# Performance work log

Measured on AMD Instinct MI355X. Metric: run time of the kernel, lower is better.

The kernel has to match this reference:

```python
import jax, jax.numpy as jnp
import numpy as np

P = 16         # patch size
D = 192        # embed dim (vit_tiny)
NH = 3         # heads
DEPTH = 12
HID = 768      # mlp hidden = 4*D
NCLS = 1000
PCT = 0.25
EPS = 1e-6


def _ln(x, s, b):
    m = x.mean(-1, keepdims=True)
    v = ((x - m) ** 2).mean(-1, keepdims=True)
    return (x - m) * jax.lax.rsqrt(v + EPS) * s + b


def setup_inputs() -> dict:
    key = jax.random.key(0)
    ks = jax.random.split(key, 24)
    B, IMG = 64, 384
    std = 0.02
    d = {
        "magno_image": jax.random.normal(ks[0], (B, 3, IMG, IMG), jnp.float32),
        "line_drawing": jax.random.uniform(ks[1], (B, 1, IMG, IMG), jnp.float32),
        "conv_w": jax.random.normal(ks[2], (D, 3, P, P), jnp.float32) * std,
        "conv_b": jnp.zeros((D,), jnp.float32),
        "pos_embed": jax.random.normal(ks[3], (1, (IMG // P) ** 2 + 1, D), jnp.float32) * std,
        "cls_token": jax.random.normal(ks[4], (1, 1, D), jnp.float32) * std,
        "ln1_s": jnp.ones((DEPTH, D), jnp.float32),
        "ln1_b": jnp.zeros((DEPTH, D), jnp.float32),
        "qkv_w": jax.random.normal(ks[5], (DEPTH, D, 3 * D), jnp.float32) * std,
        "qkv_b": jnp.zeros((DEPTH, 3 * D), jnp.float32),
        "proj_w": jax.random.normal(ks[6], (DEPTH, D, D), jnp.float32) * std,
        "proj_b": jnp.zeros((DEPTH, D), jnp.float32),
        "ln2_s": jnp.ones((DEPTH, D), jnp.float32),
        "ln2_b": jnp.zeros((DEPTH, D), jnp.float32),
        "fc1_w": jax.random.normal(ks[7], (DEPTH, D, HID), jnp.float32) * std,
        "fc1_b": jnp.zeros((DEPTH, HID), jnp.float32),
        "fc2_w": jax.random.normal(ks[8], (DEPTH, HID, D), jnp.float32) * std,
        "fc2_b": jnp.zeros((DEPTH, D), jnp.float32),
        "normf_s": jnp.ones((D,), jnp.float32),
        "normf_b": jnp.zeros((D,), jnp.float32),
        "head_w": jax.random.normal(ks[9], (D, NCLS), jnp.float32) * std,
        "head_b": jnp.zeros((NCLS,), jnp.float32),
    }
    return d


def _forward(magno_image, line_drawing, conv_w, conv_b, pos_embed, cls_token,
             ln1_s, ln1_b, qkv_w, qkv_b, proj_w, proj_b, ln2_s, ln2_b,
             fc1_w, fc1_b, fc2_w, fc2_b, normf_s, normf_b, head_w, head_b):
    B, _, IMG, _ = magno_image.shape
    g = IMG // P
    N = g * g
    k = int(N * PCT)
    hd = D // NH

    # --- PatchImportanceScorer: avg-pool(patch_size) then flatten ---
    scores = line_drawing.reshape(B, g, P, g, P).mean(axis=(2, 4)).reshape(B, N)

    # --- patch embed (conv stride == kernel == reshaped matmul) ---
    x = magno_image.reshape(B, 3, g, P, g, P).transpose(0, 2, 4, 1, 3, 5)
    patches = x.reshape(B, N, 3 * P * P) @ conv_w.reshape(D, 3 * P * P).T + conv_b

    # --- top_k selection + gather of patches and pos-embed ---
    _, idx = jax.lax.top_k(scores, k)                      # (B, k)
    sel = jnp.take_along_axis(patches, idx[:, :, None], axis=1)
    pos = jnp.take_along_axis(
        jnp.broadcast_to(pos_embed[:, 1:, :], (B, N, D)), idx[:, :, None], axis=1)
    sel = sel + pos

    cls = jnp.broadcast_to(cls_token + pos_embed[:, :1, :], (B, 1, D))
    seq = jnp.concatenate([cls, sel], axis=1)              # (B, 1+k, D)
    S = 1 + k

    def block(h, p):
        l1s, l1b, qw, qb, pw, pb, l2s, l2b, f1w, f1b, f2w, f2b = p
        y = _ln(h, l1s, l1b)
        qkv = (y @ qw + qb).reshape(B, S, 3, NH, hd)
        q, kk, v = qkv[:, :, 0], qkv[:, :, 1], qkv[:, :, 2]  # (B,S,NH,hd)
        att = jnp.einsum('bqhd,bkhd->bhqk', q, kk) / np.sqrt(hd).astype(np.float32)
        att = jax.nn.softmax(att, axis=-1)
        o = jnp.einsum('bhqk,bkhd->bqhd', att, v).reshape(B, S, D)
        h = h + o @ pw + pb
        y = _ln(h, l2s, l2b)
        h = h + jax.nn.gelu(y @ f1w + f1b, approximate=False) @ f2w + f2b
        return h, None

    seq, _ = jax.lax.scan(block, seq, (ln1_s, ln1_b, qkv_w, qkv_b, proj_w, proj_b,
                                       ln2_s, ln2_b, fc1_w, fc1_b, fc2_w, fc2_b))
    seq = _ln(seq, normf_s, normf_b)
    return seq[:, 0] @ head_w + head_b


def reference(magno_image, line_drawing, conv_w, conv_b, pos_embed, cls_token,
              ln1_s, ln1_b, qkv_w, qkv_b, proj_w, proj_b, ln2_s, ln2_b,
              fc1_w, fc1_b, fc2_w, fc2_b, normf_s, normf_b, head_w, head_b):
    return _forward(magno_image, line_drawing, conv_w, conv_b, pos_embed, cls_token,
                    ln1_s, ln1_b, qkv_w, qkv_b, proj_w, proj_b, ln2_s, ln2_b,
                    fc1_w, fc1_b, fc2_w, fc2_b, normf_s, normf_b, head_w, head_b)
```

## Files before the change

### kernel.cpp

```cpp
#include <hip/hip_runtime.h>
#include <hip/hip_bf16.h>
#include <cmath>


#define Bsz   64
#define NPATCH 576
#define KSEL  144
#define SEQ   145
#define DIM   192
#define HIDN  768

typedef __bf16 bf16x8 __attribute__((ext_vector_type(8)));
typedef float  f32x4  __attribute__((ext_vector_type(4)));

__global__ __launch_bounds__(256) void scores_kernel(const float* __restrict__ line,
                                                     float* __restrict__ scores)
{
    int gp = blockIdx.x;
    int b = gp / NPATCH, p = gp % NPATCH;
    int gy = p / 24, gx = p % 24;
    int t = threadIdx.x, py = t >> 4, px = t & 15;
    float v = line[((size_t)b * 384 + gy * 16 + py) * 384 + gx * 16 + px];
    for (int off = 32; off; off >>= 1) v += __shfl_xor(v, off);
    __shared__ float red[4];
    if ((t & 63) == 0) red[t >> 6] = v;
    __syncthreads();
    if (t == 0) scores[gp] = (red[0] + red[1] + red[2] + red[3]) * (1.f / 256.f);
}

__global__ __launch_bounds__(256) void topk_kernel(const float* __restrict__ scores,
                                                   int* __restrict__ idx)
{
    int b = blockIdx.x;
    __shared__ float s[NPATCH];
    for (int i = threadIdx.x; i < NPATCH; i += 256) s[i] = scores[b * NPATCH + i];
    __syncthreads();
    for (int i = threadIdx.x; i < NPATCH; i += 256) {
        float si = s[i];
        int cnt = 0;
        for (int j = 0; j < NPATCH; ++j) {
            float sj = s[j];
            cnt += (sj > si) || (sj == si && j < i);
        }
        if (cnt < KSEL) idx[b * KSEL + cnt] = i;
    }
}

__global__ __launch_bounds__(256) void gather_kernel(const float* __restrict__ magno,
                                                     const int* __restrict__ idx,
                                                     __hip_bfloat16* __restrict__ selp)
{
    int bs = blockIdx.x;
    int b = bs / KSEL;
    int pi = idx[bs];
    int gy = pi / 24, gx = pi % 24;
    int t = threadIdx.x, py = t >> 4, px = t & 15;
    size_t src = ((size_t)b * 3 * 384 + gy * 16 + py) * 384 + gx * 16 + px;
    __hip_bfloat16* dst = &selp[(size_t)bs * 768];
#pragma unroll
    for (int c = 0; c < 3; ++c)
        dst[c * 256 + t] = __float2bfloat16(magno[src + (size_t)c * 384 * 384]);
}

__global__ __launch_bounds__(256) void convert_bf16_kernel(const float* __restrict__ src,
                                                           __hip_bfloat16* __restrict__ dst,
                                                           int n)
{
    int i = blockIdx.x * 256 + threadIdx.x;
    if (i < n) dst[i] = __float2bfloat16(src[i]);
}

__global__ __launch_bounds__(256) void transpose_w_kernel(const float* __restrict__ src,
                                                          __hip_bfloat16* __restrict__ dst,
                                                          int R, int C)
{
    __shared__ float t[32][33];
    size_t lo = (size_t)blockIdx.z * R * C;
    int r0 = blockIdx.y * 32, c0 = blockIdx.x * 32;
    int tx = threadIdx.x & 31, ty = threadIdx.x >> 5;
#pragma unroll
    for (int i = 0; i < 32; i += 8)
        t[ty + i][tx] = src[lo + (size_t)(r0 + ty + i) * C + c0 + tx];
    __syncthreads();
#pragma unroll
    for (int i = 0; i < 32; i += 8)
        dst[lo + (size_t)(c0 + ty + i) * R + r0 + tx] = __float2bfloat16(t[tx][ty + i]);
}

__global__ void cls_kernel(const float* __restrict__ cls, const float* __restrict__ pos,
                           float* __restrict__ h)
{
    int b = blockIdx.x, t = threadIdx.x;
    h[(size_t)b * SEQ * DIM + t] = cls[t] + pos[t];
}

__global__ __launch_bounds__(256) void ln_kernel(const float* __restrict__ x,
                                                 const float* __restrict__ s,
                                                 const float* __restrict__ bia,
                                                 __hip_bfloat16* __restrict__ y, int ntok)
{
    int w = threadIdx.x >> 6, lane = threadIdx.x & 63;
    int tok = blockIdx.x * 4 + w;
    if (tok >= ntok) return;
    const float* xp = &x[(size_t)tok * DIM];
    float x0 = xp[lane], x1 = xp[lane + 64], x2 = xp[lane + 128];
    float sum = x0 + x1 + x2;
    for (int off = 32; off; off >>= 1) sum += __shfl_xor(sum, off);
    float mean = sum * (1.f / 192.f);
    float d0 = x0 - mean, d1 = x1 - mean, d2 = x2 - mean;
    float vs = d0 * d0 + d1 * d1 + d2 * d2;
    for (int off = 32; off; off >>= 1) vs += __shfl_xor(vs, off);
    float rs = rsqrtf(vs * (1.f / 192.f) + 1e-6f);
    __hip_bfloat16* yp = &y[(size_t)tok * DIM];
    yp[lane]       = __float2bfloat16(d0 * rs * s[lane]       + bia[lane]);
    yp[lane + 64]  = __float2bfloat16(d1 * rs * s[lane + 64]  + bia[lane + 64]);
    yp[lane + 128] = __float2bfloat16(d2 * rs * s[lane + 128] + bia[lane + 128]);
}

template <int MODE>
__global__ __launch_bounds__(256) void gemm_bf16(const __hip_bfloat16* __restrict__ A,
                                                 const __hip_bfloat16* __restrict__ Wt,
                                                 const float* __restrict__ bias,
                                                 void* __restrict__ Cout,
                                                 int M, int N, int K,
                                                 const int* __restrict__ selidx,
                                                 const float* __restrict__ pos)
{
    __shared__ __align__(16) char As[8192];
    __shared__ __align__(16) char Bs[8192];
    const int tid = threadIdx.x;
    const int lane = tid & 63, wid = tid >> 6;
    const int wr = wid >> 1, wc = wid & 1;
    const int lr = lane & 15, lk = lane >> 4;
    const int m0 = blockIdx.y * 64, n0 = blockIdx.x * 64;
    f32x4 acc[2][2] = {};

    for (int k0 = 0; k0 < K; k0 += 64) {
#pragma unroll
        for (int it = 0; it < 2; ++it) {
            int chunk = it * 256 + tid;
            int r = chunk >> 3, g = chunk & 7;
            int loff = r * 128 + ((g ^ (r & 7)) * 16);
            *reinterpret_cast<uint4*>(As + loff) =
                *reinterpret_cast<const uint4*>(&A[(size_t)(m0 + r) * K + k0 + g * 8]);
            *reinterpret_cast<uint4*>(Bs + loff) =
                *reinterpret_cast<const uint4*>(&Wt[(size_t)(n0 + r) * K + k0 + g * 8]);
        }
        __syncthreads();
#pragma unroll
        for (int kc = 0; kc < 2; ++kc) {
            int g = kc * 4 + lk;
            bf16x8 af[2], bfr[2];
#pragma unroll
            for (int mi = 0; mi < 2; ++mi) {
                int r = wr * 32 + mi * 16 + lr;
                af[mi] = *reinterpret_cast<const bf16x8*>(As + r * 128 + ((g ^ (r & 7)) * 16));
            }
#pragma unroll
            for (int ni = 0; ni < 2; ++ni) {
                int r = wc * 32 + ni * 16 + lr;
                bfr[ni] = *reinterpret_cast<const bf16x8*>(Bs + r * 128 + ((g ^ (r & 7)) * 16));
            }
#pragma unroll
            for (int mi = 0; mi < 2; ++mi)
#pragma unroll
                for (int ni = 0; ni < 2; ++ni)
                    acc[mi][ni] = __builtin_amdgcn_mfma_f32_16x16x32_bf16(
                        af[mi], bfr[ni], acc[mi][ni], 0, 0, 0);
        }
        __syncthreads();
    }

#pragma unroll
    for (int mi = 0; mi < 2; ++mi)
#pragma unroll
    for (int ni = 0; ni < 2; ++ni)
#pragma unroll
    for (int j = 0; j < 4; ++j) {
        int row = m0 + wr * 32 + mi * 16 + (lane >> 4) * 4 + j;
        int col = n0 + wc * 32 + ni * 16 + (lane & 15);
        float v = acc[mi][ni][j] + bias[col];
        if (MODE == 2) {
            ((__hip_bfloat16*)Cout)[(size_t)row * N + col] =
                __float2bfloat16(0.5f * v * (1.f + erff(v * 0.70710678118654752f)));
        } else {
            int bb2 = row / KSEL, ss = row % KSEL;
            int pi = selidx[row];
            v += pos[(size_t)(1 + pi) * DIM + col];
            ((float*)Cout)[((size_t)bb2 * SEQ + 1 + ss) * DIM + col] = v;
        }
    }
}

__global__ __launch_bounds__(256) void gemm_qkv(const __hip_bfloat16* __restrict__ A,
                                                const __hip_bfloat16* __restrict__ Wt,
                                                const float* __restrict__ bias,
                                                __hip_bfloat16* __restrict__ qk,
                                                __hip_bfloat16* __restrict__ Vt)
{
    __shared__ __align__(16) char As[8192];
    __shared__ __align__(16) char Bs[8192];
    const int tid = threadIdx.x;
    const int lane = tid & 63, wid = tid >> 6;
    const int wr = wid >> 1, wc = wid & 1;
    const int lr = lane & 15, lk = lane >> 4;
    const int m0 = blockIdx.y * 64, n0 = blockIdx.x * 64;
    const int K = DIM;
    f32x4 acc[2][2] = {};

    for (int k0 = 0; k0 < K; k0 += 64) {
#pragma unroll
        for (int it = 0; it < 2; ++it) {
            int chunk = it * 256 + tid;
            int r = chunk >> 3, g = chunk & 7;
            int loff = r * 128 + ((g ^ (r & 7)) * 16);
            *reinterpret_cast<uint4*>(As + loff) =
                *reinterpret_cast<const uint4*>(&A[(size_t)(m0 + r) * K + k0 + g * 8]);
            *reinterpret_cast<uint4*>(Bs + loff) =
                *reinterpret_cast<const uint4*>(&Wt[(size_t)(n0 + r) * K + k0 + g * 8]);
        }
        __syncthreads();
#pragma unroll
        for (int kc = 0; kc < 2; ++kc) {
            int g = kc * 4 + lk;
            bf16x8 af[2], bfr[2];
#pragma unroll
            for (int mi = 0; mi < 2; ++mi) {
                int r = wr * 32 + mi * 16 + lr;
                af[mi] = *reinterpret_cast<const bf16x8*>(As + r * 128 + ((g ^ (r & 7)) * 16));
            }
#pragma unroll
            for (int ni = 0; ni < 2; ++ni) {
                int r = wc * 32 + ni * 16 + lr;
                bfr[ni] = *reinterpret_cast<const bf16x8*>(Bs + r * 128 + ((g ^ (r & 7)) * 16));
            }
#pragma unroll
            for (int mi = 0; mi < 2; ++mi)
#pragma unroll
                for (int ni = 0; ni < 2; ++ni)
                    acc[mi][ni] = __builtin_amdgcn_mfma_f32_16x16x32_bf16(
                        af[mi], bfr[ni], acc[mi][ni], 0, 0, 0);
        }
        __syncthreads();
    }

#pragma unroll
    for (int mi = 0; mi < 2; ++mi)
#pragma unroll
    for (int ni = 0; ni < 2; ++ni)
#pragma unroll
    for (int j = 0; j < 4; ++j) {
        int row = m0 + wr * 32 + mi * 16 + (lane >> 4) * 4 + j;
        int col = n0 + wc * 32 + ni * 16 + (lane & 15);
        float v = acc[mi][ni][j] + bias[col];
        if (col < 384) {
            qk[(size_t)row * 384 + col] = __float2bfloat16(v);
        } else {
            int c = col - 384;
            int b = row / SEQ, s = row - b * SEQ;
            Vt[((size_t)(b * 3 + (c >> 6)) * 64 + (c & 63)) * 160 + s] = __float2bfloat16(v);
        }
    }
}

__global__ __launch_bounds__(512) void attnproj_kernel(const __hip_bfloat16* __restrict__ qk,
                                                       const __hip_bfloat16* __restrict__ Vt,
                                                       const __hip_bfloat16* __restrict__ Wp,
                                                       const float* __restrict__ pbias,
                                                       float* __restrict__ h,
                                                       const float* __restrict__ ls,
                                                       const float* __restrict__ lb,
                                                       __hip_bfloat16* __restrict__ y)
{
    const int b = blockIdx.y, qt = blockIdx.x;
    const int tid = threadIdx.x;
    const int w = tid >> 6, lane = tid & 63;
    const int lr = lane & 15, lg = lane >> 4;
    __shared__ __hip_bfloat16 Ps[3][32][168];
    __shared__ __hip_bfloat16 Ot[32][200];
    __shared__ float redsum[4][32];
    __shared__ float redsq[4][32];

    const size_t qbase = (size_t)b * SEQ * 384;
    const int q0 = qt * 32;

    if (w < 6) {
        const int hh = w >> 1, half = w & 1;
        const int qrow = q0 + half * 16;
        bf16x8 aq[2];
#pragma unroll
        for (int ks = 0; ks < 2; ++ks)
            aq[ks] = *reinterpret_cast<const bf16x8*>(
                &qk[qbase + (size_t)(qrow + lr) * 384 + hh * 64 + ks * 32 + lg * 8]);
        f32x4 sc[10] = {};
#pragma unroll
        for (int nf = 0; nf < 10; ++nf) {
            int key = nf * 16 + lr;
#pragma unroll
            for (int ks = 0; ks < 2; ++ks) {
                bf16x8 bk = *reinterpret_cast<const bf16x8*>(
                    &qk[qbase + (size_t)key * 384 + 192 + hh * 64 + ks * 32 + lg * 8]);
                sc[nf] = __builtin_amdgcn_mfma_f32_16x16x32_bf16(aq[ks], bk, sc[nf], 0, 0, 0);
            }
        }
        float mx[4] = {-1e30f, -1e30f, -1e30f, -1e30f};
#pragma unroll
        for (int nf = 0; nf < 10; ++nf) {
            bool valid = nf * 16 + lr < SEQ;
#pragma unroll
            for (int j = 0; j < 4; ++j) {
                float v = valid ? sc[nf][j] * 0.125f : -1e30f;
                sc[nf][j] = v;
                mx[j] = fmaxf(mx[j], v);
            }
        }
#pragma unroll
        for (int j = 0; j < 4; ++j)
            for (int off = 1; off < 16; off <<= 1)
                mx[j] = fmaxf(mx[j], __shfl_xor(mx[j], off));
        float sm[4] = {0.f, 0.f, 0.f, 0.f};
#pragma unroll
        for (int nf = 0; nf < 10; ++nf)
#pragma unroll
            for (int j = 0; j < 4; ++j) {
                float p = __expf(sc[nf][j] - mx[j]);
                sc[nf][j] = p;
                sm[j] += p;
            }
#pragma unroll
        for (int j = 0; j < 4; ++j) {
            for (int off = 1; off < 16; off <<= 1) sm[j] += __shfl_xor(sm[j], off);
            sm[j] = 1.f / sm[j];
        }
#pragma unroll
        for (int nf = 0; nf < 10; ++nf) {
            int key = nf * 16 + lr;
#pragma unroll
            for (int j = 0; j < 4; ++j)
                Ps[hh][half * 16 + lg * 4 + j][key] = __float2bfloat16(sc[nf][j] * sm[j]);
        }
        const __hip_bfloat16* vtb = &Vt[(size_t)(b * 3 + hh) * 64 * 160];
        f32x4 oacc[4] = {};
#pragma unroll
        for (int ks = 0; ks < 5; ++ks) {
            bf16x8 ap = *reinterpret_cast<const bf16x8*>(&Ps[hh][half * 16 + lr][ks * 32 + lg * 8]);
#pragma unroll
            for (int nf = 0; nf < 4; ++nf) {
                bf16x8 bv = *reinterpret_cast<const bf16x8*>(
                    &vtb[(size_t)(nf * 16 + lr) * 160 + ks * 32 + lg * 8]);
                oacc[nf] = __builtin_amdgcn_mfma_f32_16x16x32_bf16(ap, bv, oacc[nf], 0, 0, 0);
            }
        }
#pragma unroll
        for (int nf = 0; nf < 4; ++nf)
#pragma unroll
            for (int j = 0; j < 4; ++j)
                Ot[half * 16 + lg * 4 + j][hh * 64 + nf * 16 + lr] =
                    __float2bfloat16(oacc[nf][j]);
    }
    __syncthreads();

    const int wm = w & 1, wn = w >> 1;
    f32x4 pacc[3] = {};
#pragma unroll
    for (int kk = 0; kk < 6; ++kk) {
        bf16x8 af = *reinterpret_cast<const bf16x8*>(&Ot[wm * 16 + lr][kk * 32 + lg * 8]);
#pragma unroll
        for (int nf = 0; nf < 3; ++nf) {
            int ncol = wn * 48 + nf * 16 + lr;
            bf16x8 bw = *reinterpret_cast<const bf16x8*>(&Wp[(size_t)ncol * 192 + kk * 32 + lg * 8]);
            pacc[nf] = __builtin_amdgcn_mfma_f32_16x16x32_bf16(af, bw, pacc[nf], 0, 0, 0);
        }
    }
    float v[3][4];
    float psum[4] = {}, psq[4] = {};
#pragma unroll
    for (int nf = 0; nf < 3; ++nf) {
        int col = wn * 48 + nf * 16 + lr;
        float bcol = pbias[col];
#pragma unroll
        for (int j = 0; j < 4; ++j) {
            int q = q0 + wm * 16 + lg * 4 + j;
            float res = (q < SEQ) ? h[((size_t)b * SEQ + q) * DIM + col] : 0.f;
            float t = pacc[nf][j] + bcol + res;
            v[nf][j] = t;
            psum[j] += t;
            psq[j] += t * t;
        }
    }
#pragma unroll
    for (int j = 0; j < 4; ++j) {
        for (int off = 1; off < 16; off <<= 1) {
            psum[j] += __shfl_xor(psum[j], off);
            psq[j]  += __shfl_xor(psq[j], off);
        }
        if (lr == 0) {
            redsum[wn][wm * 16 + lg * 4 + j] = psum[j];
            redsq[wn][wm * 16 + lg * 4 + j]  = psq[j];
        }
    }
    __syncthreads();
#pragma unroll
    for (int j = 0; j < 4; ++j) {
        int r = wm * 16 + lg * 4 + j;
        int q = q0 + r;
        if (q >= SEQ) continue;
        float tsum = redsum[0][r] + redsum[1][r] + redsum[2][r] + redsum[3][r];
        float tsq  = redsq[0][r]  + redsq[1][r]  + redsq[2][r]  + redsq[3][r];
        float mean = tsum * (1.f / 192.f);
        float var  = tsq * (1.f / 192.f) - mean * mean;
        float rs = rsqrtf(var + 1e-6f);
#pragma unroll
        for (int nf = 0; nf < 3; ++nf) {
            int col = wn * 48 + nf * 16 + lr;
            float t = v[nf][j];
            h[((size_t)b * SEQ + q) * DIM + col] = t;
            y[((size_t)b * SEQ + q) * DIM + col] =
                __float2bfloat16((t - mean) * rs * ls[col] + lb[col]);
        }
    }
}

template <bool DO_LN>
__global__ __launch_bounds__(512) void gemm_res_ln(const __hip_bfloat16* __restrict__ A,
                                                   const __hip_bfloat16* __restrict__ Wt,
                                                   const float* __restrict__ bias,
                                                   float* __restrict__ h,
                                                   const float* __restrict__ ls,
                                                   const float* __restrict__ lb,
                                                   __hip_bfloat16* __restrict__ y,
                                                   int K)
{
    __shared__ __align__(16) char As[16384];
    __shared__ __align__(16) char Bs[49152];
    __shared__ float redsum[4][64];
    __shared__ float redsq[4][64];
    const int tid = threadIdx.x;
    const int lane = tid & 63, w = tid >> 6;
    const int wm = w & 1, wn = w >> 1;
    const int lr = lane & 15, lg = lane >> 4;
    const int m0 = blockIdx.x * 64;
    f32x4 acc[2][3] = {};

    for (int k0 = 0; k0 < K; k0 += 128) {
#pragma unroll
        for (int it = 0; it < 2; ++it) {
            int chunk = it * 512 + tid;
            int r = chunk >> 4, g = chunk & 15;
            *reinterpret_cast<uint4*>(As + r * 256 + ((g ^ (r & 15)) * 16)) =
                *reinterpret_cast<const uint4*>(&A[(size_t)(m0 + r) * K + k0 + g * 8]);
        }
#pragma unroll
        for (int it = 0; it < 6; ++it) {
            int chunk = it * 512 + tid;
            int r = chunk >> 4, g = chunk & 15;
            *reinterpret_cast<uint4*>(Bs + r * 256 + ((g ^ (r & 15)) * 16)) =
                *reinterpret_cast<const uint4*>(&Wt[(size_t)r * K + k0 + g * 8]);
        }
        __syncthreads();
#pragma unroll
        for (int kc = 0; kc < 4; ++kc) {
            int g = kc * 4 + lg;
            bf16x8 af[2];
#pragma unroll
            for (int mi = 0; mi < 2; ++mi) {
                int r = wm * 32 + mi * 16 + lr;
                af[mi] = *reinterpret_cast<const bf16x8*>(As + r * 256 + ((g ^ (r & 15)) * 16));
            }
#pragma unroll
            for (int nf = 0; nf < 3; ++nf) {
                int br = wn * 48 + nf * 16 + lr;
                bf16x8 bw = *reinterpret_cast<const bf16x8*>(Bs + br * 256 + ((g ^ (br & 15)) * 16));
#pragma unroll
                for (int mi = 0; mi < 2; ++mi)
                    acc[mi][nf] = __builtin_amdgcn_mfma_f32_16x16x32_bf16(
                        af[mi], bw, acc[mi][nf], 0, 0, 0);
            }
        }
        __syncthreads();
    }

    float v[2][3][4];
    float psum[2][4] = {}, psq[2][4] = {};
#pragma unroll
    for (int mi = 0; mi < 2; ++mi)
#pragma unroll
    for (int nf = 0; nf < 3; ++nf) {
        int col = wn * 48 + nf * 16 + lr;
        float bcol = bias[col];
#pragma unroll
        for (int j = 0; j < 4; ++j) {
            int row = m0 + wm * 32 + mi * 16 + lg * 4 + j;
            float t = acc[mi][nf][j] + bcol + h[(size_t)row * DIM + col];
            v[mi][nf][j] = t;
            psum[mi][j] += t;
            psq[mi][j] += t * t;
        }
    }
    if (DO_LN) {
#pragma unroll
        for (int mi = 0; mi < 2; ++mi)
#pragma unroll
            for (int j = 0; j < 4; ++j) {
                for (int off = 1; off < 16; off <<= 1) {
                    psum[mi][j] += __shfl_xor(psum[mi][j], off);
                    psq[mi][j]  += __shfl_xor(psq[mi][j], off);
                }
                if (lr == 0) {
                    redsum[wn][wm * 32 + mi * 16 + lg * 4 + j] = psum[mi][j];
                    redsq[wn][wm * 32 + mi * 16 + lg * 4 + j]  = psq[mi][j];
                }
            }
        __syncthreads();
#pragma unroll
        for (int mi = 0; mi < 2; ++mi)
#pragma unroll
            for (int j = 0; j < 4; ++j) {
                int r = wm * 32 + mi * 16 + lg * 4 + j;
                int row = m0 + r;
                float tsum = redsum[0][r] + redsum[1][r] + redsum[2][r] + redsum[3][r];
                float tsq  = redsq[0][r]  + redsq[1][r]  + redsq[2][r]  + redsq[3][r];
                float mean = tsum * (1.f / 192.f);
                float var  = tsq * (1.f / 192.f) - mean * mean;
                float rs = rsqrtf(var + 1e-6f);
#pragma unroll
                for (int nf = 0; nf < 3; ++nf) {
                    int col = wn * 48 + nf * 16 + lr;
                    float t = v[mi][nf][j];
                    h[(size_t)row * DIM + col] = t;
                    y[(size_t)row * DIM + col] =
                        __float2bfloat16((t - mean) * rs * ls[col] + lb[col]);
                }
            }
    } else {
#pragma unroll
        for (int mi = 0; mi < 2; ++mi)
#pragma unroll
        for (int nf = 0; nf < 3; ++nf) {
            int col = wn * 48 + nf * 16 + lr;
#pragma unroll
            for (int j = 0; j < 4; ++j) {
                int row = m0 + wm * 32 + mi * 16 + lg * 4 + j;
                h[(size_t)row * DIM + col] = v[mi][nf][j];
            }
        }
    }
}

__global__ __launch_bounds__(256) void head_kernel(const float* __restrict__ h,
                                                   const float* __restrict__ nfs,
                                                   const float* __restrict__ nfb,
                                                   const float* __restrict__ hw,
                                                   const float* __restrict__ hb,
                                                   float* __restrict__ out)
{
    int b = blockIdx.x, t = threadIdx.x;
    __shared__ float y[DIM];
    __shared__ float red[4];
    float x = (t < DIM) ? h[(size_t)b * SEQ * DIM + t] : 0.f;
    float sum = x;
    for (int off = 32; off; off >>= 1) sum += __shfl_xor(sum, off);
    if ((t & 63) == 0) red[t >> 6] = sum;
    __syncthreads();
    float mean = (red[0] + red[1] + red[2] + red[3]) * (1.f / 192.f);
    __syncthreads();
    float d = (t < DIM) ? (x - mean) : 0.f;
    float v = d * d;
    for (int off = 32; off; off >>= 1) v += __shfl_xor(v, off);
    if ((t & 63) == 0) red[t >> 6] = v;
    __syncthreads();
    float var = (red[0] + red[1] + red[2] + red[3]) * (1.f / 192.f);
    float rs = rsqrtf(var + 1e-6f);
    if (t < DIM) y[t] = d * rs * nfs[t] + nfb[t];
    __syncthreads();
    for (int n = t; n < 1000; n += 256) {
        float acc = hb[n];
#pragma unroll 8
        for (int k = 0; k < DIM; ++k)
            acc = fmaf(y[k], hw[(size_t)k * 1000 + n], acc);
        out[(size_t)b * 1000 + n] = acc;
    }
}

extern "C" void kernel_launch(void* const* d_in, const int* in_sizes, int n_in,
                              void* d_out, int out_size, void* d_ws, size_t ws_size,
                              hipStream_t stream)
{
    const float* magno  = (const float*)d_in[0];
    const float* line   = (const float*)d_in[1];
    const float* conv_w = (const float*)d_in[2];
    const float* conv_b = (const float*)d_in[3];
    const float* pos    = (const float*)d_in[4];
    const float* cls    = (const float*)d_in[5];
    const float* ln1_s  = (const float*)d_in[6];
    const float* ln1_b  = (const float*)d_in[7];
    const float* qkv_w  = (const float*)d_in[8];
    const float* qkv_b  = (const float*)d_in[9];
    const float* proj_w = (const float*)d_in[10];
    const float* proj_b = (const float*)d_in[11];
    const float* ln2_s  = (const float*)d_in[12];
    const float* ln2_b  = (const float*)d_in[13];
    const float* fc1_w  = (const float*)d_in[14];
    const float* fc1_b  = (const float*)d_in[15];
    const float* fc2_w  = (const float*)d_in[16];
    const float* fc2_b  = (const float*)d_in[17];
    const float* normf_s = (const float*)d_in[18];
    const float* normf_b = (const float*)d_in[19];
    const float* head_w = (const float*)d_in[20];
    const float* head_b = (const float*)d_in[21];
    float* out = (float*)d_out;
    (void)in_sizes; (void)n_in; (void)out_size; (void)ws_size;

    char* ws = (char*)d_ws;
    int*            idx     = (int*)            (ws + 0);
    float*          h       = (float*)          (ws + 147456);
    __hip_bfloat16* y       = (__hip_bfloat16*) (ws + 7274496);
    __hip_bfloat16* qk      = (__hip_bfloat16*) (ws + 10838016);
    __hip_bfloat16* Vt      = (__hip_bfloat16*) (ws + 17965056);
    __hip_bfloat16* tbuf    = (__hip_bfloat16*) (ws + 21897216);
    __hip_bfloat16* wt_qkv  = (__hip_bfloat16*) (ws + 36151296);
    __hip_bfloat16* wt_proj = (__hip_bfloat16*) (ws + 38805504);
    __hip_bfloat16* wt_fc1  = (__hip_bfloat16*) (ws + 39690240);
    __hip_bfloat16* wt_fc2  = (__hip_bfloat16*) (ws + 43229184);
    float*          scoresbuf = (float*)qk;
    __hip_bfloat16* convT     = y;
    __hip_bfloat16* selp      = tbuf;

    hipMemsetAsync(Vt, 0, 3932160, stream);
    transpose_w_kernel<<<dim3(18, 6, 12), 256, 0, stream>>>(qkv_w, wt_qkv, DIM, 576);
    transpose_w_kernel<<<dim3(6, 6, 12),  256, 0, stream>>>(proj_w, wt_proj, DIM, DIM);
    transpose_w_kernel<<<dim3(24, 6, 12), 256, 0, stream>>>(fc1_w, wt_fc1, DIM, HIDN);
    transpose_w_kernel<<<dim3(6, 24, 12), 256, 0, stream>>>(fc2_w, wt_fc2, HIDN, DIM);
    convert_bf16_kernel<<<576, 256, 0, stream>>>(conv_w, convT, DIM * 768);

    scores_kernel<<<Bsz * NPATCH, 256, 0, stream>>>(line, scoresbuf);
    topk_kernel<<<Bsz, 256, 0, stream>>>(scoresbuf, idx);
    gather_kernel<<<Bsz * KSEL, 256, 0, stream>>>(magno, idx, selp);
    cls_kernel<<<Bsz, DIM, 0, stream>>>(cls, pos, h);
    gemm_bf16<3><<<dim3(3, 144), 256, 0, stream>>>(selp, convT, conv_b, h,
                                                   9216, DIM, 768, idx, pos);

    const int ntok = Bsz * SEQ;
    ln_kernel<<<ntok / 4, 256, 0, stream>>>(h, ln1_s, ln1_b, y, ntok);
    for (int l = 0; l < 12; ++l) {
        gemm_qkv<<<dim3(9, 145), 256, 0, stream>>>(y, wt_qkv + (size_t)l * 576 * DIM,
                                                   qkv_b + l * 576, qk, Vt);
        attnproj_kernel<<<dim3(5, Bsz), 512, 0, stream>>>(qk, Vt,
                                                          wt_proj + (size_t)l * DIM * DIM,
                                                          proj_b + l * DIM, h,
                                                          ln2_s + l * DIM, ln2_b + l * DIM, y);
        gemm_bf16<2><<<dim3(12, 145), 256, 0, stream>>>(y, wt_fc1 + (size_t)l * HIDN * DIM,
                                                        fc1_b + l * HIDN, tbuf,
                                                        ntok, HIDN, DIM, nullptr, nullptr);
        if (l < 11)
            gemm_res_ln<true><<<145, 512, 0, stream>>>(
                tbuf, wt_fc2 + (size_t)l * DIM * HIDN, fc2_b + l * DIM, h,
                ln1_s + (l + 1) * DIM, ln1_b + (l + 1) * DIM, y, HIDN);
        else
            gemm_res_ln<false><<<145, 512, 0, stream>>>(
                tbuf, wt_fc2 + (size_t)l * DIM * HIDN, fc2_b + l * DIM, h,
                nullptr, nullptr, y, HIDN);
    }
    head_kernel<<<Bsz, 256, 0, stream>>>(h, normf_s, normf_b, head_w, head_b, out);
}
```

Baseline: 967.3 us.

## Fuse FC1+GELU into attention-projection kernel and restructure FC2 residual-LN GEMM

The post-attention LayerNorm output now stays in shared memory, and each attention block runs the FC1 GEMM and GELU directly, writing the hidden activations. This removes a kernel launch and the round trip of y through global memory. In exchange only 320 blocks do the FC1 work, reading B fragments straight from global memory instead of staging them in LDS. The FC2 residual-LN kernel moves from 512 to 256 threads. Each wave now owns full rows, so the LN reduction uses shuffles only and a two-pass variance, with no shared-memory reduction.

```diff
diff --git a/kernel.cpp b/kernel.cpp
--- a/kernel.cpp
+++ b/kernel.cpp
@@ -117,14 +117,13 @@
     yp[lane + 128] = __float2bfloat16(d2 * rs * s[lane + 128] + bia[lane + 128]);
 }
 
-template <int MODE>
-__global__ __launch_bounds__(256) void gemm_bf16(const __hip_bfloat16* __restrict__ A,
-                                                 const __hip_bfloat16* __restrict__ Wt,
-                                                 const float* __restrict__ bias,
-                                                 void* __restrict__ Cout,
-                                                 int M, int N, int K,
-                                                 const int* __restrict__ selidx,
-                                                 const float* __restrict__ pos)
+__global__ __launch_bounds__(256) void gemm_embed(const __hip_bfloat16* __restrict__ A,
+                                                  const __hip_bfloat16* __restrict__ Wt,
+                                                  const float* __restrict__ bias,
+                                                  float* __restrict__ h,
+                                                  int K,
+                                                  const int* __restrict__ selidx,
+                                                  const float* __restrict__ pos)
 {
     __shared__ __align__(16) char As[8192];
     __shared__ __align__(16) char Bs[8192];
@@ -180,15 +179,10 @@
         int row = m0 + wr * 32 + mi * 16 + (lane >> 4) * 4 + j;
         int col = n0 + wc * 32 + ni * 16 + (lane & 15);
         float v = acc[mi][ni][j] + bias[col];
-        if (MODE == 2) {
-            ((__hip_bfloat16*)Cout)[(size_t)row * N + col] =
-                __float2bfloat16(0.5f * v * (1.f + erff(v * 0.70710678118654752f)));
-        } else {
-            int bb2 = row / KSEL, ss = row % KSEL;
-            int pi = selidx[row];
-            v += pos[(size_t)(1 + pi) * DIM + col];
-            ((float*)Cout)[((size_t)bb2 * SEQ + 1 + ss) * DIM + col] = v;
-        }
+        int bb2 = row / KSEL, ss = row % KSEL;
+        int pi = selidx[row];
+        v += pos[(size_t)(1 + pi) * DIM + col];
+        h[((size_t)bb2 * SEQ + 1 + ss) * DIM + col] = v;
     }
 }
 
@@ -263,14 +257,17 @@
     }
 }
 
-__global__ __launch_bounds__(512) void attnproj_kernel(const __hip_bfloat16* __restrict__ qk,
-                                                       const __hip_bfloat16* __restrict__ Vt,
-                                                       const __hip_bfloat16* __restrict__ Wp,
-                                                       const float* __restrict__ pbias,
-                                                       float* __restrict__ h,
-                                                       const float* __restrict__ ls,
-                                                       const float* __restrict__ lb,
-                                                       __hip_bfloat16* __restrict__ y)
+__global__ __launch_bounds__(512) void attnproj_fc1_kernel(
+    const __hip_bfloat16* __restrict__ qk,
+    const __hip_bfloat16* __restrict__ Vt,
+    const __hip_bfloat16* __restrict__ Wp,
+    const float* __restrict__ pbias,
+    float* __restrict__ h,
+    const float* __restrict__ ls,
+    const float* __restrict__ lb,
+    const __hip_bfloat16* __restrict__ W1t,
+    const float* __restrict__ b1,
+    __hip_bfloat16* __restrict__ tbuf)
 {
     const int b = blockIdx.y, qt = blockIdx.x;
     const int tid = threadIdx.x;
@@ -280,6 +277,7 @@
     __shared__ __hip_bfloat16 Ot[32][200];
     __shared__ float redsum[4][32];
     __shared__ float redsq[4][32];
+    __hip_bfloat16* Yt = &Ps[0][0][0];
 
     const size_t qbase = (size_t)b * SEQ * 384;
     const int q0 = qt * 32;
@@ -404,7 +402,6 @@
     for (int j = 0; j < 4; ++j) {
         int r = wm * 16 + lg * 4 + j;
         int q = q0 + r;
-        if (q >= SEQ) continue;
         float tsum = redsum[0][r] + redsum[1][r] + redsum[2][r] + redsum[3][r];
         float tsq  = redsq[0][r]  + redsq[1][r]  + redsq[2][r]  + redsq[3][r];
         float mean = tsum * (1.f / 192.f);
@@ -414,15 +411,50 @@
         for (int nf = 0; nf < 3; ++nf) {
             int col = wn * 48 + nf * 16 + lr;
             float t = v[nf][j];
-            h[((size_t)b * SEQ + q) * DIM + col] = t;
-            y[((size_t)b * SEQ + q) * DIM + col] =
-                __float2bfloat16((t - mean) * rs * ls[col] + lb[col]);
+            float yv = (t - mean) * rs * ls[col] + lb[col];
+            Yt[r * 200 + col] = __float2bfloat16(yv);
+            if (q < SEQ) h[((size_t)b * SEQ + q) * DIM + col] = t;
+        }
+    }
+    __syncthreads();
+
+    f32x4 facc[2][6] = {};
+#pragma unroll
+    for (int ks = 0; ks < 6; ++ks) {
+        bf16x8 af[2];
+#pragma unroll
+        for (int mi = 0; mi < 2; ++mi)
+            af[mi] = *reinterpret_cast<const bf16x8*>(&Yt[(mi * 16 + lr) * 200 + ks * 32 + lg * 8]);
+#pragma unroll
+        for (int nf = 0; nf < 6; ++nf) {
+            int col = w * 96 + nf * 16 + lr;
+            bf16x8 bw = *reinterpret_cast<const bf16x8*>(&W1t[(size_t)col * DIM + ks * 32 + lg * 8]);
+#pragma unroll
+            for (int mi = 0; mi < 2; ++mi)
+                facc[mi][nf] = __builtin_amdgcn_mfma_f32_16x16x32_bf16(
+                    af[mi], bw, facc[mi][nf], 0, 0, 0);
+        }
+    }
+#pragma unroll
+    for (int mi = 0; mi < 2; ++mi)
+#pragma unroll
+    for (int nf = 0; nf < 6; ++nf) {
+        int col = w * 96 + nf * 16 + lr;
+        float bcol = b1[col];
+#pragma unroll
+        for (int j = 0; j < 4; ++j) {
+            int q = q0 + mi * 16 + lg * 4 + j;
+            if (q < SEQ) {
+                float vv = facc[mi][nf][j] + bcol;
+                float ge = 0.5f * vv * (1.f + erff(vv * 0.70710678118654752f));
+                tbuf[((size_t)b * SEQ + q) * HIDN + col] = __float2bfloat16(ge);
+            }
         }
     }
 }
 
 template <bool DO_LN>
-__global__ __launch_bounds__(512) void gemm_res_ln(const __hip_bfloat16* __restrict__ A,
+__global__ __launch_bounds__(256) void gemm_res_ln(const __hip_bfloat16* __restrict__ A,
                                                    const __hip_bfloat16* __restrict__ Wt,
                                                    const float* __restrict__ bias,
                                                    float* __restrict__ h,
@@ -431,117 +463,91 @@
                                                    __hip_bfloat16* __restrict__ y,
                                                    int K)
 {
-    __shared__ __align__(16) char As[16384];
-    __shared__ __align__(16) char Bs[49152];
-    __shared__ float redsum[4][64];
-    __shared__ float redsq[4][64];
+    __shared__ __align__(16) char As[8192];
+    __shared__ __align__(16) char Bs[24576];
     const int tid = threadIdx.x;
     const int lane = tid & 63, w = tid >> 6;
-    const int wm = w & 1, wn = w >> 1;
     const int lr = lane & 15, lg = lane >> 4;
     const int m0 = blockIdx.x * 64;
-    f32x4 acc[2][3] = {};
-
-    for (int k0 = 0; k0 < K; k0 += 128) {
-#pragma unroll
-        for (int it = 0; it < 2; ++it) {
-            int chunk = it * 512 + tid;
-            int r = chunk >> 4, g = chunk & 15;
-            *reinterpret_cast<uint4*>(As + r * 256 + ((g ^ (r & 15)) * 16)) =
-                *reinterpret_cast<const uint4*>(&A[(size_t)(m0 + r) * K + k0 + g * 8]);
-        }
-#pragma unroll
-        for (int it = 0; it < 6; ++it) {
-            int chunk = it * 512 + tid;
-            int r = chunk >> 4, g = chunk & 15;
-            *reinterpret_cast<uint4*>(Bs + r * 256 + ((g ^ (r & 15)) * 16)) =
-                *reinterpret_cast<const uint4*>(&Wt[(size_t)r * K + k0 + g * 8]);
+    f32x4 acc[12] = {};
+
+    for (int k0 = 0; k0 < K; k0 += 64) {
+        {
+            int chunk = tid;
+#pragma unroll
+            for (int it = 0; it < 2; ++it, chunk += 256) {
+                int r = chunk >> 3, g = chunk & 7;
+                *reinterpret_cast<uint4*>(As + r * 128 + ((g ^ (r & 7)) * 16)) =
+                    *reinterpret_cast<const uint4*>(&A[(size_t)(m0 + r) * K + k0 + g * 8]);
+            }
+        }
+        {
+            int chunk = tid;
+#pragma unroll
+            for (int it = 0; it < 6; ++it, chunk += 256) {
+                int r = chunk >> 3, g = chunk & 7;
+                *reinterpret_cast<uint4*>(Bs + r * 128 + ((g ^ (r & 7)) * 16)) =
+                    *reinterpret_cast<const uint4*>(&Wt[(size_t)r * K + k0 + g * 8]);
+            }
         }
         __syncthreads();
 #pragma unroll
-        for (int kc = 0; kc < 4; ++kc) {
+        for (int kc = 0; kc < 2; ++kc) {
             int g = kc * 4 + lg;
-            bf16x8 af[2];
-#pragma unroll
-            for (int mi = 0; mi < 2; ++mi) {
-                int r = wm * 32 + mi * 16 + lr;
-                af[mi] = *reinterpret_cast<const bf16x8*>(As + r * 256 + ((g ^ (r & 15)) * 16));
-            }
-#pragma unroll
-            for (int nf = 0; nf < 3; ++nf) {
-                int br = wn * 48 + nf * 16 + lr;
-                bf16x8 bw = *reinterpret_cast<const bf16x8*>(Bs + br * 256 + ((g ^ (br & 15)) * 16));
-#pragma unroll
-                for (int mi = 0; mi < 2; ++mi)
-                    acc[mi][nf] = __builtin_amdgcn_mfma_f32_16x16x32_bf16(
-                        af[mi], bw, acc[mi][nf], 0, 0, 0);
+            int ar = w * 16 + lr;
+            bf16x8 af = *reinterpret_cast<const bf16x8*>(As + ar * 128 + ((g ^ (ar & 7)) * 16));
+#pragma unroll
+            for (int nf = 0; nf < 12; ++nf) {
+                int br = nf * 16 + lr;
+                bf16x8 bfv = *reinterpret_cast<const bf16x8*>(Bs + br * 128 + ((g ^ (br & 7)) * 16));
+                acc[nf] = __builtin_amdgcn_mfma_f32_16x16x32_bf16(af, bfv, acc[nf], 0, 0, 0);
             }
         }
         __syncthreads();
     }
 
-    float v[2][3][4];
-    float psum[2][4] = {}, psq[2][4] = {};
-#pragma unroll
-    for (int mi = 0; mi < 2; ++mi)
-#pragma unroll
-    for (int nf = 0; nf < 3; ++nf) {
-        int col = wn * 48 + nf * 16 + lr;
-        float bcol = bias[col];
+    float v[12][4];
+    float sum[4] = {0.f, 0.f, 0.f, 0.f};
+#pragma unroll
+    for (int nf = 0; nf < 12; ++nf) {
+        int col = nf * 16 + lr;
 #pragma unroll
         for (int j = 0; j < 4; ++j) {
-            int row = m0 + wm * 32 + mi * 16 + lg * 4 + j;
-            float t = acc[mi][nf][j] + bcol + h[(size_t)row * DIM + col];
-            v[mi][nf][j] = t;
-            psum[mi][j] += t;
-            psq[mi][j] += t * t;
+            int row = m0 + w * 16 + lg * 4 + j;
+            float t = acc[nf][j] + bias[col] + h[(size_t)row * DIM + col];
+            v[nf][j] = t;
+            h[(size_t)row * DIM + col] = t;
+            sum[j] += t;
         }
     }
     if (DO_LN) {
 #pragma unroll
-        for (int mi = 0; mi < 2; ++mi)
+        for (int j = 0; j < 4; ++j)
+            for (int off = 1; off < 16; off <<= 1) sum[j] += __shfl_xor(sum[j], off);
+        float mean[4], sq[4] = {0.f, 0.f, 0.f, 0.f};
+#pragma unroll
+        for (int j = 0; j < 4; ++j) mean[j] = sum[j] * (1.f / 192.f);
+#pragma unroll
+        for (int nf = 0; nf < 12; ++nf)
 #pragma unroll
             for (int j = 0; j < 4; ++j) {
-                for (int off = 1; off < 16; off <<= 1) {
-                    psum[mi][j] += __shfl_xor(psum[mi][j], off);
-                    psq[mi][j]  += __shfl_xor(psq[mi][j], off);
-                }
-                if (lr == 0) {
-                    redsum[wn][wm * 32 + mi * 16 + lg * 4 + j] = psum[mi][j];
-                    redsq[wn][wm * 32 + mi * 16 + lg * 4 + j]  = psq[mi][j];
-                }
-            }
-        __syncthreads();
-#pragma unroll
-        for (int mi = 0; mi < 2; ++mi)
+                float d = v[nf][j] - mean[j];
+                sq[j] += d * d;
+            }
+#pragma unroll
+        for (int j = 0; j < 4; ++j) {
+            for (int off = 1; off < 16; off <<= 1) sq[j] += __shfl_xor(sq[j], off);
+            sq[j] = rsqrtf(sq[j] * (1.f / 192.f) + 1e-6f);
+        }
+#pragma unroll
+        for (int nf = 0; nf < 12; ++nf) {
+            int col = nf * 16 + lr;
+            float sc = ls[col], bc = lb[col];
 #pragma unroll
             for (int j = 0; j < 4; ++j) {
-                int r = wm * 32 + mi * 16 + lg * 4 + j;
-                int row = m0 + r;
-                float tsum = redsum[0][r] + redsum[1][r] + redsum[2][r] + redsum[3][r];
-                float tsq  = redsq[0][r]  + redsq[1][r]  + redsq[2][r]  + redsq[3][r];
-                float mean = tsum * (1.f / 192.f);
-                float var  = tsq * (1.f / 192.f) - mean * mean;
-                float rs = rsqrtf(var + 1e-6f);
-#pragma unroll
-                for (int nf = 0; nf < 3; ++nf) {
-                    int col = wn * 48 + nf * 16 + lr;
-                    float t = v[mi][nf][j];
-                    h[(size_t)row * DIM + col] = t;
-                    y[(size_t)row * DIM + col] =
-                        __float2bfloat16((t - mean) * rs * ls[col] + lb[col]);
-                }
-            }
-    } else {
-#pragma unroll
-        for (int mi = 0; mi < 2; ++mi)
-#pragma unroll
-        for (int nf = 0; nf < 3; ++nf) {
-            int col = wn * 48 + nf * 16 + lr;
-#pragma unroll
-            for (int j = 0; j < 4; ++j) {
-                int row = m0 + wm * 32 + mi * 16 + lg * 4 + j;
-                h[(size_t)row * DIM + col] = v[mi][nf][j];
+                int row = m0 + w * 16 + lg * 4 + j;
+                y[(size_t)row * DIM + col] =
+                    __float2bfloat16((v[nf][j] - mean[j]) * sq[j] * sc + bc);
             }
         }
     }
@@ -637,27 +643,24 @@
     topk_kernel<<<Bsz, 256, 0, stream>>>(scoresbuf, idx);
     gather_kernel<<<Bsz * KSEL, 256, 0, stream>>>(magno, idx, selp);
     cls_kernel<<<Bsz, DIM, 0, stream>>>(cls, pos, h);
-    gemm_bf16<3><<<dim3(3, 144), 256, 0, stream>>>(selp, convT, conv_b, h,
-                                                   9216, DIM, 768, idx, pos);
+    gemm_embed<<<dim3(3, 144), 256, 0, stream>>>(selp, convT, conv_b, h,
+                                                 768, idx, pos);
 
     const int ntok = Bsz * SEQ;
     ln_kernel<<<ntok / 4, 256, 0, stream>>>(h, ln1_s, ln1_b, y, ntok);
     for (int l = 0; l < 12; ++l) {
         gemm_qkv<<<dim3(9, 145), 256, 0, stream>>>(y, wt_qkv + (size_t)l * 576 * DIM,
                                                    qkv_b + l * 576, qk, Vt);
-        attnproj_kernel<<<dim3(5, Bsz), 512, 0, stream>>>(qk, Vt,
-                                                          wt_proj + (size_t)l * DIM * DIM,
-                                                          proj_b + l * DIM, h,
-                                                          ln2_s + l * DIM, ln2_b + l * DIM, y);
-        gemm_bf16<2><<<dim3(12, 145), 256, 0, stream>>>(y, wt_fc1 + (size_t)l * HIDN * DIM,
-                                                        fc1_b + l * HIDN, tbuf,
-                                                        ntok, HIDN, DIM, nullptr, nullptr);
+        attnproj_fc1_kernel<<<dim3(5, Bsz), 512, 0, stream>>>(
+            qk, Vt, wt_proj + (size_t)l * DIM * DIM, proj_b + l * DIM, h,
+            ln2_s + l * DIM, ln2_b + l * DIM,
+            wt_fc1 + (size_t)l * HIDN * DIM, fc1_b + l * HIDN, tbuf);
         if (l < 11)
-            gemm_res_ln<true><<<145, 512, 0, stream>>>(
+            gemm_res_ln<true><<<145, 256, 0, stream>>>(
                 tbuf, wt_fc2 + (size_t)l * DIM * HIDN, fc2_b + l * DIM, h,
                 ln1_s + (l + 1) * DIM, ln1_b + (l + 1) * DIM, y, HIDN);
         else
-            gemm_res_ln<false><<<145, 512, 0, stream>>>(
+            gemm_res_ln<false><<<145, 256, 0, stream>>>(
                 tbuf, wt_fc2 + (size_t)l * DIM * HIDN, fc2_b + l * DIM, h,
                 nullptr, nullptr, y, HIDN);
     }
```

Result: slower. 1.140 ms (+17.8%).
